# Kernel optimization log

Measured on AMD Instinct MI355X. Metric: run time of the kernel, lower is better.

The kernel has to match this reference:

```python
import jax, jax.numpy as jnp
import numpy as np

D_MODEL = 1024
D_STATE = 16
D_CONV = 4
EXPAND = 2
D_INNER = D_MODEL * EXPAND


def setup_inputs() -> dict:
    key = jax.random.key(0)
    ks = jax.random.split(key, 8)
    B, L = 2, 2048
    x = jax.random.normal(ks[0], (B, L, D_MODEL), dtype=jnp.float32)
    # in_proj: Linear(d_model -> 2*d_inner), no bias
    W_in = jax.random.normal(ks[1], (D_MODEL, 2 * D_INNER), dtype=jnp.float32) / np.sqrt(D_MODEL)
    # depthwise conv1d: (d_inner, 1, d_conv) + bias
    conv_w = jax.random.normal(ks[2], (D_INNER, 1, D_CONV), dtype=jnp.float32) / np.sqrt(D_CONV)
    conv_b = jax.random.normal(ks[3], (D_INNER,), dtype=jnp.float32) * 0.01
    # x_proj: Linear(d_inner -> 2*d_state + 1), no bias
    W_x = jax.random.normal(ks[4], (D_INNER, 2 * D_STATE + 1), dtype=jnp.float32) / np.sqrt(D_INNER)
    # A_log ~ Uniform(-log(d_state), -1)
    A_log = jax.random.uniform(ks[5], (D_INNER, D_STATE), dtype=jnp.float32,
                               minval=-np.log(D_STATE), maxval=-1.0)
    D_param = jnp.ones((D_INNER,), dtype=jnp.float32)
    W_out = jax.random.normal(ks[6], (D_INNER, D_MODEL), dtype=jnp.float32) / np.sqrt(D_INNER)
    return {"x": x, "W_in": W_in, "conv_w": conv_w, "conv_b": conv_b,
            "W_x": W_x, "A_log": A_log, "D_param": D_param, "W_out": W_out}


def _selective_scan(x, delta, A, Bm, Cm):
    # x:(B,L,D), delta:(B,L), A:(D,N), Bm/Cm:(B,L,N)
    Bsz, L, Dd = x.shape
    N = A.shape[1]
    h0 = jnp.zeros((Bsz, Dd, N), dtype=x.dtype)

    def step(h, inp):
        dt, Bt, Ct, xt = inp  # (B,), wait dt:(B,), Bt:(B,N), Ct:(B,N), xt:(B,D)
        A_bar = jnp.exp(dt[:, None, None] * A)          # (B,D,N)
        dB = (dt[:, None] * Bt)[:, None, :]             # (B,1,N)
        h = A_bar * h + dB * xt[:, :, None]             # (B,D,N)
        y = jnp.einsum('bn,bdn->bd', Ct, h)             # (B,D)
        return h, y

    xs = (jnp.swapaxes(delta, 0, 1), jnp.swapaxes(Bm, 0, 1),
          jnp.swapaxes(Cm, 0, 1), jnp.swapaxes(x, 0, 1))
    _, ys = jax.lax.scan(step, h0, xs)                  # ys: (L,B,D)
    return jnp.swapaxes(ys, 0, 1)


def reference(x, W_in, conv_w, conv_b, W_x, A_log, D_param, W_out):
    B, L, _ = x.shape
    xr = x @ W_in                                       # (B,L,2*Di)
    x_inner, res = jnp.split(xr, 2, axis=-1)
    # causal depthwise conv: left-pad d_conv-1, valid conv == torch slice [:L]
    xc = jnp.swapaxes(x_inner, 1, 2)                    # (B,Di,L)
    xc = jax.lax.conv_general_dilated(
        xc, conv_w, window_strides=(1,), padding=[(D_CONV - 1, 0)],
        dimension_numbers=('NCH', 'OIH', 'NCH'), feature_group_count=D_INNER)
    xc = xc + conv_b[None, :, None]
    xc = jnp.swapaxes(xc, 1, 2)                         # (B,L,Di)
    xc = jax.nn.silu(xc)
    ssm_params = xc @ W_x                               # (B,L,1+2N)
    delta = jax.nn.softplus(ssm_params[..., 0])         # (B,L)
    Bm = ssm_params[..., 1:1 + D_STATE]                 # (B,L,N)
    Cm = ssm_params[..., 1 + D_STATE:]                  # (B,L,N)
    A = -jnp.exp(A_log)                                 # (Di,N)
    y = _selective_scan(xc, delta, A, Bm, Cm)           # (B,L,Di)
    y = y + xc * D_param[None, None, :]
    y = y * jax.nn.silu(res)
    return y @ W_out                                    # (B,L,d_model)
```

## Files before the change

kernel.cpp:

```cpp
#include <hip/hip_runtime.h>

#define L_SEQ 2048
#define NB    2
#define DMOD  1024
#define DIN   2048
#define NST   16
#define NROWS (NB*L_SEQ)
#define CL    64
#define NC    (L_SEQ/CL)

typedef unsigned short u16;
typedef _Float16 half8 __attribute__((ext_vector_type(8)));
typedef float f32x4 __attribute__((ext_vector_type(4)));
typedef short short8 __attribute__((ext_vector_type(8)));

__device__ __forceinline__ float siluf(float v){ return v / (1.f + __expf(-v)); }
__device__ __forceinline__ u16 f2h_bits(float v){ _Float16 h = (_Float16)v; return __builtin_bit_cast(u16, h); }
__device__ __forceinline__ float h2f(u16 v){ return (float)__builtin_bit_cast(_Float16, v); }
__device__ __forceinline__ float fexp2(float x){
#if __has_builtin(__builtin_amdgcn_exp2f)
    return __builtin_amdgcn_exp2f(x);
#else
    return __expf(x * 0.69314718056f);
#endif
}

__device__ __forceinline__ void gload16(const u16* g, u16* l)
{
    __builtin_amdgcn_global_load_lds(
        (const __attribute__((address_space(1))) void*)g,
        (__attribute__((address_space(3))) void*)l,
        16, 0, 0);
}

#define BARRIER() do { asm volatile("" ::: "memory"); __builtin_amdgcn_s_barrier(); asm volatile("" ::: "memory"); } while (0)
#define VMCNT2()  asm volatile("s_waitcnt vmcnt(2)" ::: "memory")

__global__ __launch_bounds__(256)
void prep_inputs(const float* __restrict__ x, const float* __restrict__ W_in,
                 const float* __restrict__ W_out, const float* __restrict__ Wx,
                 u16* __restrict__ x16, u16* __restrict__ Bt1,
                 u16* __restrict__ Bt3, u16* __restrict__ WxT16)
{
    __shared__ float s[64][65];
    const int bid = blockIdx.x, tid = threadIdx.x;
    if (bid < 4096) {
        int i = bid * 256 + tid;
        float4 v = ((const float4*)x)[i];
        ushort4 o;
        o.x = f2h_bits(v.x); o.y = f2h_bits(v.y); o.z = f2h_bits(v.z); o.w = f2h_bits(v.w);
        *(ushort4*)&x16[(size_t)i * 4] = o;
    } else if (bid < 5632) {
        const float* in; u16* outT; int R, C, rblk, cblk;
        if (bid < 5120) { int b = bid - 4096; in = W_in;  outT = Bt1; R = 1024; C = 4096; cblk = b & 63; rblk = b >> 6; }
        else            { int b = bid - 5120; in = W_out; outT = Bt3; R = 2048; C = 1024; cblk = b & 15; rblk = b >> 4; }
        int r0 = rblk * 64, c0 = cblk * 64;
        int tc = tid & 63, ty = tid >> 6;
        #pragma unroll
        for (int j = 0; j < 16; j++) {
            int r = ty + j * 4;
            s[r][tc] = in[(size_t)(r0 + r) * C + c0 + tc];
        }
        __syncthreads();
        #pragma unroll
        for (int j = 0; j < 16; j++) {
            int nn = ty + j * 4;
            outT[(size_t)(c0 + nn) * R + r0 + tc] = f2h_bits(s[tc][nn]);
        }
    } else {
        int idx = (bid - 5632) * 256 + tid;
        int n = idx >> 11, k = idx & 2047;
        float v = (n < 33) ? Wx[k * 33 + n] : 0.f;
        WxT16[idx] = f2h_bits(v);
    }
}

template<int EPI>
__global__ __launch_bounds__(512, 2)
void gemm8(const u16* __restrict__ A, const u16* __restrict__ Bt,
           void* __restrict__ C0v, void* __restrict__ C1v,
           int M, int N, int KLEN, int lda, int ldb)
{
    __shared__ __align__(16) u16 As[2 * 256 * 64];
    __shared__ __align__(16) u16 Bs[2 * 256 * 64];
    const int tid  = threadIdx.x;
    const int lane = tid & 63;
    const int w    = tid >> 6;
    const int wm   = w >> 2, wn = w & 3;
    const int bm = blockIdx.y * 256, bn = blockIdx.x * 256;
    const int kBase = blockIdx.z * KLEN;

    const int srow8 = lane >> 3;
    const int sunit = (lane & 7) ^ srow8;
    const u16* Ag = A  + (size_t)(bm + srow8) * lda + kBase + sunit * 8;
    const u16* Bg = Bt + (size_t)(bn + srow8) * ldb + kBase + sunit * 8;
    const int rw = w * 16;

    const int fr  = lane & 15;
    const int sl0 = ((lane >> 4) ^ (fr & 7)) * 8;
    int aOffs[8], bOffs[4];
    #pragma unroll
    for (int mi = 0; mi < 8; mi++) aOffs[mi] = (wm * 128 + mi * 16 + fr) * 64 + sl0;
    #pragma unroll
    for (int ni = 0; ni < 4; ni++) bOffs[ni] = (ni * 64 + wn * 16 + fr) * 64 + sl0;

    f32x4 acc[8][4];
    #pragma unroll
    for (int i = 0; i < 8; i++)
        #pragma unroll
        for (int j = 0; j < 4; j++)
            acc[i][j] = (f32x4){0.f, 0.f, 0.f, 0.f};

    auto stage2 = [&](const u16* G, int ld, int rbase, int kcol, u16* ldsDst) {
        gload16(G + (size_t)rbase * ld + kcol, ldsDst);
        gload16(G + (size_t)(rbase + 8) * ld + kcol, ldsDst + 8 * 64);
    };

    const int NT = KLEN >> 6;
    stage2(Ag, lda, 0 + rw, 0, &As[(0 + rw) * 64]);
    stage2(Ag, lda, 128 + rw, 0, &As[(128 + rw) * 64]);
    stage2(Bg, ldb, 0 + rw, 0, &Bs[(0 + rw) * 64]);
    stage2(Bg, ldb, 128 + rw, 0, &Bs[(128 + rw) * 64]);
    VMCNT2();
    BARRIER();

    for (int t = 0; t < NT; ++t) {
        const int cO = (t & 1) << 14;
        const int nO = cO ^ 16384;
        const int kn = (t + 1) << 6;
        const bool pf = (t + 1) < NT;
        half8 af[8], bf0, bf1;

        #pragma unroll
        for (int mi = 0; mi < 8; mi++) af[mi] = *(const half8*)&As[cO + aOffs[mi]];
        bf0 = *(const half8*)&Bs[cO + bOffs[0]];
        bf1 = *(const half8*)&Bs[cO + bOffs[1]];
        if (pf) stage2(Ag, lda, 0 + rw, kn, &As[nO + (0 + rw) * 64]);
        BARRIER();
        #pragma unroll
        for (int mi = 0; mi < 8; mi++) acc[mi][0] = __builtin_amdgcn_mfma_f32_16x16x32_f16(af[mi], bf0, acc[mi][0], 0, 0, 0);
        #pragma unroll
        for (int mi = 0; mi < 8; mi++) acc[mi][1] = __builtin_amdgcn_mfma_f32_16x16x32_f16(af[mi], bf1, acc[mi][1], 0, 0, 0);
        VMCNT2();
        BARRIER();

        bf0 = *(const half8*)&Bs[cO + bOffs[2]];
        bf1 = *(const half8*)&Bs[cO + bOffs[3]];
        if (pf) stage2(Ag, lda, 128 + rw, kn, &As[nO + (128 + rw) * 64]);
        BARRIER();
        #pragma unroll
        for (int mi = 0; mi < 8; mi++) acc[mi][2] = __builtin_amdgcn_mfma_f32_16x16x32_f16(af[mi], bf0, acc[mi][2], 0, 0, 0);
        #pragma unroll
        for (int mi = 0; mi < 8; mi++) acc[mi][3] = __builtin_amdgcn_mfma_f32_16x16x32_f16(af[mi], bf1, acc[mi][3], 0, 0, 0);
        BARRIER();

        #pragma unroll
        for (int mi = 0; mi < 8; mi++) af[mi] = *(const half8*)&As[cO + (aOffs[mi] ^ 32)];
        bf0 = *(const half8*)&Bs[cO + (bOffs[0] ^ 32)];
        bf1 = *(const half8*)&Bs[cO + (bOffs[1] ^ 32)];
        if (pf) stage2(Bg, ldb, 0 + rw, kn, &Bs[nO + (0 + rw) * 64]);
        BARRIER();
        #pragma unroll
        for (int mi = 0; mi < 8; mi++) acc[mi][0] = __builtin_amdgcn_mfma_f32_16x16x32_f16(af[mi], bf0, acc[mi][0], 0, 0, 0);
        #pragma unroll
        for (int mi = 0; mi < 8; mi++) acc[mi][1] = __builtin_amdgcn_mfma_f32_16x16x32_f16(af[mi], bf1, acc[mi][1], 0, 0, 0);
        BARRIER();

        bf0 = *(const half8*)&Bs[cO + (bOffs[2] ^ 32)];
        bf1 = *(const half8*)&Bs[cO + (bOffs[3] ^ 32)];
        if (pf) stage2(Bg, ldb, 128 + rw, kn, &Bs[nO + (128 + rw) * 64]);
        BARRIER();
        #pragma unroll
        for (int mi = 0; mi < 8; mi++) acc[mi][2] = __builtin_amdgcn_mfma_f32_16x16x32_f16(af[mi], bf0, acc[mi][2], 0, 0, 0);
        #pragma unroll
        for (int mi = 0; mi < 8; mi++) acc[mi][3] = __builtin_amdgcn_mfma_f32_16x16x32_f16(af[mi], bf1, acc[mi][3], 0, 0, 0);
        VMCNT2();
        BARRIER();
    }

    const int cr = (lane >> 4) * 4;
    #pragma unroll
    for (int mi = 0; mi < 8; mi++) {
        #pragma unroll
        for (int ni = 0; ni < 4; ni++) {
            #pragma unroll
            for (int q = 0; q < 4; q++) {
                int row = bm + wm * 128 + mi * 16 + cr + q;
                int col = bn + ni * 64 + wn * 16 + fr;
                float v = acc[mi][ni][q];
                if (EPI == 1) {
                    int half = N >> 1;
                    if (col < half) ((u16*)C0v)[(size_t)row * half + col] = f2h_bits(v);
                    else            ((u16*)C1v)[(size_t)row * half + col - half] = f2h_bits(siluf(v));
                } else {
                    ((u16*)C0v)[((size_t)blockIdx.z * M + row) * N + col] = f2h_bits(v);
                }
            }
        }
    }
}

__global__ __launch_bounds__(256)
void add_partials4(const u16* __restrict__ p, float* __restrict__ out)
{
    int i = blockIdx.x * 256 + threadIdx.x;
    const size_t stride = (size_t)NROWS * DMOD;
    float acc[8] = {0,0,0,0,0,0,0,0};
    #pragma unroll
    for (int z = 0; z < 4; z++) {
        short8 a = *(const short8*)&p[z * stride + (size_t)i * 8];
        #pragma unroll
        for (int j = 0; j < 8; j++) acc[j] += h2f((u16)a[j]);
    }
    float4 o0 = {acc[0], acc[1], acc[2], acc[3]};
    float4 o1 = {acc[4], acc[5], acc[6], acc[7]};
    *(float4*)&out[(size_t)i * 8]     = o0;
    *(float4*)&out[(size_t)i * 8 + 4] = o1;
}

__global__ __launch_bounds__(256)
void conv_silu16t(const u16* __restrict__ xin16, const float* __restrict__ cw,
                  const float* __restrict__ cb, u16* __restrict__ xc16)
{
    __shared__ u16 sx[35][136];
    const int d0 = blockIdx.x << 7, t0 = blockIdx.y << 5, b = blockIdx.z;
    const int tid = threadIdx.x;
    for (int i = tid; i < 35 * 16; i += 256) {
        int r = i >> 4, u = i & 15;
        int t = t0 - 3 + r;
        short8 v = {0,0,0,0,0,0,0,0};
        if (t >= 0) v = *(const short8*)&xin16[((size_t)(b * L_SEQ + t)) * DIN + d0 + u * 8];
        *(short8*)&sx[r][u * 8] = v;
    }
    __syncthreads();
    const int u  = tid & 15;
    const int tl = tid >> 4;
    const int d  = d0 + u * 8;
    const float4* cw4 = (const float4*)cw;
    float4 w[8];
    #pragma unroll
    for (int j = 0; j < 8; j++) w[j] = cw4[d + j];
    float bias[8];
    {
        float4 b0 = *(const float4*)&cb[d];
        float4 b1 = *(const float4*)&cb[d + 4];
        bias[0]=b0.x; bias[1]=b0.y; bias[2]=b0.z; bias[3]=b0.w;
        bias[4]=b1.x; bias[5]=b1.y; bias[6]=b1.z; bias[7]=b1.w;
    }
    #pragma unroll
    for (int half = 0; half < 2; half++) {
        const int t_l = tl + half * 16;
        float acc[8];
        #pragma unroll
        for (int j = 0; j < 8; j++) acc[j] = bias[j];
        #pragma unroll
        for (int k = 0; k < 4; k++) {
            short8 v = *(const short8*)&sx[t_l + k][u * 8];
            #pragma unroll
            for (int j = 0; j < 8; j++)
                acc[j] = fmaf(h2f((u16)v[j]), (&w[j].x)[k], acc[j]);
        }
        short8 o;
        #pragma unroll
        for (int j = 0; j < 8; j++) o[j] = (short)f2h_bits(siluf(acc[j]));
        *(short8*)&xc16[((size_t)(b * L_SEQ + t0 + t_l)) * DIN + d] = o;
    }
}

__global__ __launch_bounds__(256)
void gemm2_mfma(const u16* __restrict__ A, const u16* __restrict__ Bt, float* __restrict__ pb)
{
    __shared__ __align__(16) u16 As[64 * 64];
    __shared__ __align__(16) u16 Bs[48 * 64];
    const int tid = threadIdx.x, lane = tid & 63, w = tid >> 6;
    const int bm = blockIdx.x * 64;
    const int kz = blockIdx.y;
    const int arow = tid >> 2;
    const int au   = (tid & 3) << 1;
    f32x4 acc[3];
    acc[0] = acc[1] = acc[2] = (f32x4){0.f, 0.f, 0.f, 0.f};

    for (int it = 0; it < 4; ++it) {
        const int k0 = kz * 256 + it * 64;
        short8 ra0 = *(const short8*)&A[(size_t)(bm + arow) * DIN + k0 + au * 8];
        short8 ra1 = *(const short8*)&A[(size_t)(bm + arow) * DIN + k0 + (au + 1) * 8];
        short8 rb0, rb1;
        if (tid < 192) {
            rb0 = *(const short8*)&Bt[(size_t)arow * DIN + k0 + au * 8];
            rb1 = *(const short8*)&Bt[(size_t)arow * DIN + k0 + (au + 1) * 8];
        }
        __syncthreads();
        {
            int s0 = au ^ (arow & 7), s1 = (au + 1) ^ (arow & 7);
            *(short8*)&As[arow * 64 + s0 * 8] = ra0;
            *(short8*)&As[arow * 64 + s1 * 8] = ra1;
            if (tid < 192) {
                *(short8*)&Bs[arow * 64 + s0 * 8] = rb0;
                *(short8*)&Bs[arow * 64 + s1 * 8] = rb1;
            }
        }
        __syncthreads();
        #pragma unroll
        for (int kk = 0; kk < 2; kk++) {
            int r = w * 16 + (lane & 15);
            int sl = (kk * 4 + (lane >> 4)) ^ (r & 7);
            half8 af = *(const half8*)&As[r * 64 + sl * 8];
            #pragma unroll
            for (int ni = 0; ni < 3; ni++) {
                int br = ni * 16 + (lane & 15);
                int bsl = (kk * 4 + (lane >> 4)) ^ (br & 7);
                half8 bf = *(const half8*)&Bs[br * 64 + bsl * 8];
                acc[ni] = __builtin_amdgcn_mfma_f32_16x16x32_f16(af, bf, acc[ni], 0, 0, 0);
            }
        }
    }
    #pragma unroll
    for (int ni = 0; ni < 3; ni++) {
        #pragma unroll
        for (int q = 0; q < 4; q++) {
            int row = bm + w * 16 + (lane >> 4) * 4 + q;
            int col = ni * 16 + (lane & 15);
            pb[((size_t)kz * NROWS + row) * 48 + col] = acc[ni][q];
        }
    }
}

__global__ __launch_bounds__(256)
void gemm2_reduce(const float* __restrict__ pb, float* __restrict__ delta,
                  float* __restrict__ Bm, float* __restrict__ Cm)
{
    int idx = blockIdx.x * 256 + threadIdx.x;
    int row = idx / 48, col = idx - row * 48;
    float s = 0.f;
    #pragma unroll
    for (int kz = 0; kz < 8; kz++) s += pb[(size_t)kz * NROWS * 48 + idx];
    if (col == 0)       delta[row] = fmaxf(s, 0.f) + log1pf(__expf(-fabsf(s)));
    else if (col < 17)  Bm[row * NST + col - 1]  = s;
    else if (col < 33)  Cm[row * NST + col - 17] = s;
}

__global__ __launch_bounds__(256)
void scan_part1_reg(const u16* __restrict__ xc16, const float* __restrict__ delta,
                    const float* __restrict__ Bm, const float* __restrict__ A_log,
                    float* __restrict__ h_loc, float* __restrict__ Pc)
{
    const int b = blockIdx.z, c = blockIdx.y;
    const int d = blockIdx.x * 256 + threadIdx.x;
    float ka[16];
    {
        const float4* Av = (const float4*)(A_log + (size_t)d * 16);
        #pragma unroll
        for (int q = 0; q < 4; q++) {
            float4 a = Av[q];
            ka[q*4+0] = -__expf(a.x) * 1.44269504f;
            ka[q*4+1] = -__expf(a.y) * 1.44269504f;
            ka[q*4+2] = -__expf(a.z) * 1.44269504f;
            ka[q*4+3] = -__expf(a.w) * 1.44269504f;
        }
    }
    float h[16];
    #pragma unroll
    for (int n = 0; n < 16; n++) h[n] = 0.f;
    float S = 0.f;
    const int rowbase = b * L_SEQ + c * CL;
    #pragma unroll 2
    for (int t = 0; t < CL; ++t) {
        const int rowg = rowbase + t;
        const float dt = delta[rowg];
        const float4* Bv = (const float4*)(Bm + (size_t)rowg * 16);
        float4 b0 = Bv[0], b1 = Bv[1], b2 = Bv[2], b3 = Bv[3];
        float bb[16] = {b0.x,b0.y,b0.z,b0.w, b1.x,b1.y,b1.z,b1.w,
                        b2.x,b2.y,b2.z,b2.w, b3.x,b3.y,b3.z,b3.w};
        const float xt = h2f(xc16[(size_t)rowg * DIN + d]);
        const float dtx = dt * xt;
        S += dt;
        #pragma unroll
        for (int n = 0; n < 16; n++) {
            float a = fexp2(dt * ka[n]);
            h[n] = fmaf(a, h[n], bb[n] * dtx);
        }
    }
    float* hp = h_loc + (((size_t)(b * NC + c) * DIN) + d) * 16;
    float* pp = Pc    + (((size_t)(b * NC + c) * DIN) + d) * 16;
    #pragma unroll
    for (int q = 0; q < 4; q++) {
        *(float4*)&hp[q*4] = (float4){h[q*4+0], h[q*4+1], h[q*4+2], h[q*4+3]};
        *(float4*)&pp[q*4] = (float4){fexp2(S*ka[q*4+0]), fexp2(S*ka[q*4+1]),
                                      fexp2(S*ka[q*4+2]), fexp2(S*ka[q*4+3])};
    }
}

__global__ __launch_bounds__(256)
void scan_carry(const float* __restrict__ h_loc, const float* __restrict__ Pc,
                float* __restrict__ H_in)
{
    int gid = blockIdx.x * 256 + threadIdx.x;
    int b = gid >> 15, r = gid & 32767;
    float H = 0.f;
    for (int c = 0; c < NC; ++c) {
        size_t idx = ((size_t)(b * NC + c) << 15) + r;
        H_in[idx] = H;
        H = fmaf(Pc[idx], H, h_loc[idx]);
    }
}

__global__ __launch_bounds__(256)
void scan_part3_reg(const u16* __restrict__ xc16, const float* __restrict__ delta,
                    const float* __restrict__ Bm, const float* __restrict__ Cm,
                    const float* __restrict__ A_log, const float* __restrict__ Dp,
                    const u16* __restrict__ res16, const float* __restrict__ H_in,
                    u16* __restrict__ yh)
{
    const int b = blockIdx.z, c = blockIdx.y;
    const int d = blockIdx.x * 256 + threadIdx.x;
    float ka[16];
    {
        const float4* Av = (const float4*)(A_log + (size_t)d * 16);
        #pragma unroll
        for (int q = 0; q < 4; q++) {
            float4 a = Av[q];
            ka[q*4+0] = -__expf(a.x) * 1.44269504f;
            ka[q*4+1] = -__expf(a.y) * 1.44269504f;
            ka[q*4+2] = -__expf(a.z) * 1.44269504f;
            ka[q*4+3] = -__expf(a.w) * 1.44269504f;
        }
    }
    float h[16];
    {
        const float4* Hv = (const float4*)(H_in + (((size_t)(b * NC + c) * DIN) + d) * 16);
        #pragma unroll
        for (int q = 0; q < 4; q++) {
            float4 v = Hv[q];
            h[q*4+0]=v.x; h[q*4+1]=v.y; h[q*4+2]=v.z; h[q*4+3]=v.w;
        }
    }
    const float Dpd = Dp[d];
    const int rowbase = b * L_SEQ + c * CL;
    #pragma unroll 2
    for (int t = 0; t < CL; ++t) {
        const int rowg = rowbase + t;
        const float dt = delta[rowg];
        const float4* Bv = (const float4*)(Bm + (size_t)rowg * 16);
        const float4* Cv = (const float4*)(Cm + (size_t)rowg * 16);
        float4 b0 = Bv[0], b1 = Bv[1], b2 = Bv[2], b3 = Bv[3];
        float4 c0 = Cv[0], c1 = Cv[1], c2 = Cv[2], c3 = Cv[3];
        float bb[16] = {b0.x,b0.y,b0.z,b0.w, b1.x,b1.y,b1.z,b1.w,
                        b2.x,b2.y,b2.z,b2.w, b3.x,b3.y,b3.z,b3.w};
        float cc[16] = {c0.x,c0.y,c0.z,c0.w, c1.x,c1.y,c1.z,c1.w,
                        c2.x,c2.y,c2.z,c2.w, c3.x,c3.y,c3.z,c3.w};
        const float xt = h2f(xc16[(size_t)rowg * DIN + d]);
        const float rt = h2f(res16[(size_t)rowg * DIN + d]);
        const float dtx = dt * xt;
        float y = 0.f;
        #pragma unroll
        for (int n = 0; n < 16; n++) {
            float a = fexp2(dt * ka[n]);
            h[n] = fmaf(a, h[n], bb[n] * dtx);
            y = fmaf(cc[n], h[n], y);
        }
        y = (y + xt * Dpd) * rt;
        yh[(size_t)rowg * DIN + d] = f2h_bits(y);
    }
}

extern "C" void kernel_launch(void* const* d_in, const int* in_sizes, int n_in,
                              void* d_out, int out_size, void* d_ws, size_t ws_size,
                              hipStream_t stream)
{
    const float* x     = (const float*)d_in[0];
    const float* W_in  = (const float*)d_in[1];
    const float* cw    = (const float*)d_in[2];
    const float* cb    = (const float*)d_in[3];
    const float* Wx    = (const float*)d_in[4];
    const float* A_log = (const float*)d_in[5];
    const float* Dp    = (const float*)d_in[6];
    const float* W_out = (const float*)d_in[7];
    float* out = (float*)d_out;
    float* ws  = (float*)d_ws;

    u16*   xin16 = (u16*)(ws);
    u16*   y16   = (u16*)(ws);
    u16*   res16 = (u16*)(ws + 4194304);
    u16*   xc16  = (u16*)(ws + 8388608);
    u16*   x16   = (u16*)(ws + 12582912);
    u16*   p4    = (u16*)(ws + 12582912);
    u16*   Bt1   = (u16*)(ws + 14680064);
    float* pb    = ws + 14680064;
    u16*   WxT16 = (u16*)(ws + 20971520);
    float* delta = ws + 21020672;
    float* Bm    = ws + 21024768;
    float* Cm    = ws + 21090304;
    float* h_loc = ws + 21155840;
    float* Pc    = ws + 23252992;
    float* H_in  = ws + 25350144;
    u16*   Bt3   = (u16*)(ws + 27447296);

    dim3 blk(256), blk512(512);

    prep_inputs<<<dim3(6016), blk, 0, stream>>>(x, W_in, W_out, Wx, x16, Bt1, Bt3, WxT16);
    gemm8<1><<<dim3(16, 16, 1), blk512, 0, stream>>>(x16, Bt1, xin16, res16,
                                                     NROWS, 2 * DIN, DMOD, DMOD, DMOD);
    conv_silu16t<<<dim3(DIN / 128, L_SEQ / 32, NB), blk, 0, stream>>>(xin16, cw, cb, xc16);
    gemm2_mfma<<<dim3(NROWS / 64, 8), blk, 0, stream>>>(xc16, WxT16, pb);
    gemm2_reduce<<<dim3(NROWS * 48 / 256), blk, 0, stream>>>(pb, delta, Bm, Cm);
    scan_part1_reg<<<dim3(DIN / 256, NC, NB), blk, 0, stream>>>(xc16, delta, Bm, A_log, h_loc, Pc);
    scan_carry<<<dim3(NB * DIN * NST / 256), blk, 0, stream>>>(h_loc, Pc, H_in);
    scan_part3_reg<<<dim3(DIN / 256, NC, NB), blk, 0, stream>>>(xc16, delta, Bm, Cm, A_log, Dp, res16, H_in, y16);
    gemm8<2><<<dim3(DMOD / 256, NROWS / 256, 4), blk512, 0, stream>>>(y16, Bt3, p4, nullptr,
                                                                     NROWS, DMOD, DIN / 4, DIN, DIN);
    add_partials4<<<dim3(NROWS * DMOD / 8 / 256), blk, 0, stream>>>(p4, out);
}
```

Measured before the change: 188.2 us.

## Replace out-projection GEMM with 128x128 tiled kernel and 2-way split-K

```diff
diff --git a/kernel.cpp b/kernel.cpp
--- a/kernel.cpp
+++ b/kernel.cpp
@@ -34,7 +34,9 @@
 }
 
 #define BARRIER() do { asm volatile("" ::: "memory"); __builtin_amdgcn_s_barrier(); asm volatile("" ::: "memory"); } while (0)
+#define VMCNT0()  asm volatile("s_waitcnt vmcnt(0)" ::: "memory")
 #define VMCNT2()  asm volatile("s_waitcnt vmcnt(2)" ::: "memory")
+#define VMCNT8()  asm volatile("s_waitcnt vmcnt(8)" ::: "memory")
 
 __global__ __launch_bounds__(256)
 void prep_inputs(const float* __restrict__ x, const float* __restrict__ W_in,
@@ -188,32 +190,115 @@
                 int row = bm + wm * 128 + mi * 16 + cr + q;
                 int col = bn + ni * 64 + wn * 16 + fr;
                 float v = acc[mi][ni][q];
-                if (EPI == 1) {
-                    int half = N >> 1;
-                    if (col < half) ((u16*)C0v)[(size_t)row * half + col] = f2h_bits(v);
-                    else            ((u16*)C1v)[(size_t)row * half + col - half] = f2h_bits(siluf(v));
-                } else {
-                    ((u16*)C0v)[((size_t)blockIdx.z * M + row) * N + col] = f2h_bits(v);
-                }
+                int half = N >> 1;
+                if (col < half) ((u16*)C0v)[(size_t)row * half + col] = f2h_bits(v);
+                else            ((u16*)C1v)[(size_t)row * half + col - half] = f2h_bits(siluf(v));
             }
         }
     }
 }
 
-__global__ __launch_bounds__(256)
-void add_partials4(const u16* __restrict__ p, float* __restrict__ out)
+__global__ __launch_bounds__(256, 2)
+void gemm128c(const u16* __restrict__ A, const u16* __restrict__ Bt,
+              u16* __restrict__ C0, int M, int N, int KLEN, int lda, int ldb)
+{
+    __shared__ __align__(16) u16 As[2 * 128 * 64];
+    __shared__ __align__(16) u16 Bs[2 * 128 * 64];
+    const int tid  = threadIdx.x;
+    const int lane = tid & 63;
+    const int wid  = tid >> 6;
+    const int wm   = wid >> 1, wn = wid & 1;
+    const int bm = blockIdx.y * 128, bn = blockIdx.x * 128;
+    const int kBase = blockIdx.z * KLEN;
+
+    const int srow8 = lane >> 3;
+    const int sunit = (lane & 7) ^ srow8;
+    const u16* Ag = A  + (size_t)(bm + srow8) * lda + kBase + sunit * 8;
+    const u16* Bg = Bt + (size_t)(bn + srow8) * ldb + kBase + sunit * 8;
+
+    const int fr = lane & 15;
+    const int s0 = ((lane >> 4) ^ (lane & 7)) * 8;
+    const int aBase = (wm * 64 + fr) * 64 + s0;
+    const int bBase = (wn * 64 + fr) * 64 + s0;
+
+    f32x4 acc[4][4];
+    #pragma unroll
+    for (int i = 0; i < 4; i++)
+        #pragma unroll
+        for (int j = 0; j < 4; j++)
+            acc[i][j] = (f32x4){0.f, 0.f, 0.f, 0.f};
+
+    auto STAGE = [&](int bufO, int k0) {
+        #pragma unroll
+        for (int j = 0; j < 4; j++) {
+            int c = wid * 4 + j;
+            gload16(Ag + (size_t)(c * 8) * lda + k0, &As[bufO + c * 512]);
+            gload16(Bg + (size_t)(c * 8) * ldb + k0, &Bs[bufO + c * 512]);
+        }
+    };
+
+    auto COMPUTE = [&](int bufO) {
+        #pragma unroll
+        for (int kk = 0; kk < 2; kk++) {
+            const int x = kk ? 32 : 0;
+            half8 af[4], bf[4];
+            #pragma unroll
+            for (int mi = 0; mi < 4; mi++)
+                af[mi] = *(const half8*)&As[bufO + (aBase ^ x) + mi * 1024];
+            #pragma unroll
+            for (int ni = 0; ni < 4; ni++)
+                bf[ni] = *(const half8*)&Bs[bufO + (bBase ^ x) + ni * 1024];
+            #pragma unroll
+            for (int mi = 0; mi < 4; mi++)
+                #pragma unroll
+                for (int ni = 0; ni < 4; ni++)
+                    acc[mi][ni] = __builtin_amdgcn_mfma_f32_16x16x32_f16(af[mi], bf[ni], acc[mi][ni], 0, 0, 0);
+        }
+    };
+
+    const int NT = KLEN >> 6;
+    STAGE(0, 0);
+    int buf = 0;
+    for (int t = 0; t < NT; ++t) {
+        if (t + 1 < NT) { STAGE(buf ^ 8192, (t + 1) << 6); VMCNT8(); }
+        else            { VMCNT0(); }
+        BARRIER();
+        COMPUTE(buf);
+        BARRIER();
+        buf ^= 8192;
+    }
+
+    const int cr = (lane >> 4) * 4;
+    const int cc = lane & 15;
+    #pragma unroll
+    for (int mi = 0; mi < 4; mi++) {
+        #pragma unroll
+        for (int ni = 0; ni < 4; ni++) {
+            #pragma unroll
+            for (int q = 0; q < 4; q++) {
+                int row = bm + wm * 64 + mi * 16 + cr + q;
+                int col = bn + wn * 64 + ni * 16 + cc;
+                C0[((size_t)blockIdx.z * M + row) * N + col] = f2h_bits(acc[mi][ni][q]);
+            }
+        }
+    }
+}
+
+__global__ __launch_bounds__(256)
+void add_partials(const u16* __restrict__ p, float* __restrict__ out)
 {
     int i = blockIdx.x * 256 + threadIdx.x;
-    const size_t stride = (size_t)NROWS * DMOD;
-    float acc[8] = {0,0,0,0,0,0,0,0};
-    #pragma unroll
-    for (int z = 0; z < 4; z++) {
-        short8 a = *(const short8*)&p[z * stride + (size_t)i * 8];
-        #pragma unroll
-        for (int j = 0; j < 8; j++) acc[j] += h2f((u16)a[j]);
-    }
-    float4 o0 = {acc[0], acc[1], acc[2], acc[3]};
-    float4 o1 = {acc[4], acc[5], acc[6], acc[7]};
+    short8 a = *(const short8*)&p[(size_t)i * 8];
+    short8 b = *(const short8*)&p[(size_t)NROWS * DMOD + (size_t)i * 8];
+    float4 o0, o1;
+    o0.x = h2f((u16)a[0]) + h2f((u16)b[0]);
+    o0.y = h2f((u16)a[1]) + h2f((u16)b[1]);
+    o0.z = h2f((u16)a[2]) + h2f((u16)b[2]);
+    o0.w = h2f((u16)a[3]) + h2f((u16)b[3]);
+    o1.x = h2f((u16)a[4]) + h2f((u16)b[4]);
+    o1.y = h2f((u16)a[5]) + h2f((u16)b[5]);
+    o1.z = h2f((u16)a[6]) + h2f((u16)b[6]);
+    o1.w = h2f((u16)a[7]) + h2f((u16)b[7]);
     *(float4*)&out[(size_t)i * 8]     = o0;
     *(float4*)&out[(size_t)i * 8 + 4] = o1;
 }
@@ -483,7 +568,7 @@
     u16*   res16 = (u16*)(ws + 4194304);
     u16*   xc16  = (u16*)(ws + 8388608);
     u16*   x16   = (u16*)(ws + 12582912);
-    u16*   p4    = (u16*)(ws + 12582912);
+    u16*   p2    = (u16*)(ws + 12582912);
     u16*   Bt1   = (u16*)(ws + 14680064);
     float* pb    = ws + 14680064;
     u16*   WxT16 = (u16*)(ws + 20971520);
@@ -506,7 +591,7 @@
     scan_part1_reg<<<dim3(DIN / 256, NC, NB), blk, 0, stream>>>(xc16, delta, Bm, A_log, h_loc, Pc);
     scan_carry<<<dim3(NB * DIN * NST / 256), blk, 0, stream>>>(h_loc, Pc, H_in);
     scan_part3_reg<<<dim3(DIN / 256, NC, NB), blk, 0, stream>>>(xc16, delta, Bm, Cm, A_log, Dp, res16, H_in, y16);
-    gemm8<2><<<dim3(DMOD / 256, NROWS / 256, 4), blk512, 0, stream>>>(y16, Bt3, p4, nullptr,
-                                                                     NROWS, DMOD, DIN / 4, DIN, DIN);
-    add_partials4<<<dim3(NROWS * DMOD / 8 / 256), blk, 0, stream>>>(p4, out);
-}
+    gemm128c<<<dim3(DMOD / 128, NROWS / 128, 2), blk, 0, stream>>>(y16, Bt3, p2,
+                                                                   NROWS, DMOD, DIN / 2, DIN, DIN);
+    add_partials<<<dim3(NROWS * DMOD / 8 / 256), blk, 0, stream>>>(p2, out);
+}
```

Result: no change. 187.2 us (-0.6%).
